# Kernel tuning notes

Measured on AMD Instinct MI355X. Metric: run time of the kernel, lower is better.

The kernel has to match this reference:

```python
import jax, jax.numpy as jnp
import numpy as np

E = 1024  # embedding_dim
QD = 1024  # query_dim (also key dim)
VD = 1024  # value_dim
B, S = 4, 2048


def setup_inputs() -> dict:
    key = jax.random.key(0)
    k1, k2, k3, k4, k5, k6, k7, k8 = jax.random.split(key, 8)
    x = jax.random.normal(k1, (B, S, E), dtype=jnp.float32)
    mask = jax.random.randint(k2, (B, S, S), 0, 2, dtype=jnp.int32)
    s = 1.0 / np.sqrt(E)
    Wq = jax.random.uniform(k3, (E, QD), jnp.float32, -s, s)
    bq = jax.random.uniform(k4, (QD,), jnp.float32, -s, s)
    Wk = jax.random.uniform(k5, (E, QD), jnp.float32, -s, s)
    bk = jax.random.uniform(k6, (QD,), jnp.float32, -s, s)
    Wv = jax.random.uniform(k7, (E, VD), jnp.float32, -s, s)
    bv = jax.random.uniform(k8, (VD,), jnp.float32, -s, s)
    return {"x": x, "mask": mask, "Wq": Wq, "bq": bq, "Wk": Wk, "bk": bk, "Wv": Wv, "bv": bv}


def reference(x, mask, Wq, bq, Wk, bk, Wv, bv):
    # projections: [B,S,E] @ [E,D] -> [B,S,D]
    q = jnp.einsum('bse,ed->bsd', x, Wq) + bq
    k = jnp.einsum('bse,ed->bsd', x, Wk) + bk
    v = jnp.einsum('bse,ed->bsd', x, Wv) + bv
    # scores scaled by query_dim (NOT sqrt(query_dim)), per original code
    weights = jnp.einsum('bqd,bkd->bqk', q, k) / QD
    weights = jnp.where(mask == 0, -jnp.inf, weights)
    weights = jax.nn.softmax(weights, axis=-1)
    out = jnp.einsum('bqk,bkd->bqd', weights, v)
    return out
```

## Files before the change

kernel.cpp:

```cpp
#include <hip/hip_runtime.h>
#include <hip/hip_bf16.h>


typedef __bf16 bf16x8 __attribute__((ext_vector_type(8)));
typedef __bf16 bf16x4 __attribute__((ext_vector_type(4)));
typedef float f32x4 __attribute__((ext_vector_type(4)));

#define BM 128
#define BN 128
#define BK 64

__device__ inline void glds16(const __bf16* g, __bf16* l) {
    __builtin_amdgcn_global_load_lds(
        (const __attribute__((address_space(1))) unsigned int*)g,
        (__attribute__((address_space(3))) unsigned int*)l,
        16, 0, 0);
}

template <int EPI>
__global__ __launch_bounds__(256) void gemm_bt(
    const __bf16* __restrict__ A, const __bf16* __restrict__ B,
    float* __restrict__ Cf, __bf16* __restrict__ Cb,
    const float* __restrict__ bias,
    int M, int N, int K, float scale,
    long sA, long sB, long sC)
{
    A += (long)blockIdx.z * sA;
    B += (long)blockIdx.z * sB;
    if (EPI == 3) Cf += (long)blockIdx.z * sC;
    if (EPI == 4) Cb += (long)blockIdx.z * sC;

    __shared__ __align__(16) char smraw[65536];
    float* smC = (float*)smraw;

    const int t = threadIdx.x;
    const int w = t >> 6;
    const int l = t & 63;
    const int row0 = blockIdx.x * BM;
    const int col0 = blockIdx.y * BN;
    const int wm = (w >> 1) * 64;
    const int wn = (w & 1) * 64;

    const int srow = l >> 3;
    const int skel = (((l & 7) ^ srow) & 7) * 8;

    const int lm = l & 15;
    const int g16 = l >> 4;
    const int sx = lm & 7;

    f32x4 acc[4][4];
#pragma unroll
    for (int i = 0; i < 4; i++)
#pragma unroll
        for (int j = 0; j < 4; j++) acc[i][j] = (f32x4){0.f, 0.f, 0.f, 0.f};

    auto stage = [&](int buf, int kt) {
        __bf16* sA = (__bf16*)(smraw + buf * 32768);
        __bf16* sB = sA + BM * BK;
#pragma unroll
        for (int i = 0; i < 4; i++) {
            const int chunk = i * 4 + w;
            const int r = chunk * 8 + srow;
            glds16(A + (size_t)(row0 + r) * K + kt + skel, &sA[chunk * 512]);
            glds16(B + (size_t)(col0 + r) * K + kt + skel, &sB[chunk * 512]);
        }
    };

    stage(0, 0);
    int cur = 0;
    for (int kt = 0; kt < K; kt += BK) {
        __syncthreads();
        if (kt + BK < K) stage(cur ^ 1, kt + BK);

        const __bf16* sA = (const __bf16*)(smraw + cur * 32768);
        const __bf16* sB = sA + BM * BK;
#pragma unroll
        for (int ks = 0; ks < 2; ks++) {
            bf16x8 af[4], bg[4];
            const int p = ((ks * 4 + g16) ^ sx) * 8;
#pragma unroll
            for (int mt = 0; mt < 4; mt++)
                af[mt] = *(const bf16x8*)&sA[(wm + mt * 16 + lm) * BK + p];
#pragma unroll
            for (int nt = 0; nt < 4; nt++)
                bg[nt] = *(const bf16x8*)&sB[(wn + nt * 16 + lm) * BK + p];
#pragma unroll
            for (int mt = 0; mt < 4; mt++)
#pragma unroll
                for (int nt = 0; nt < 4; nt++)
                    acc[mt][nt] = __builtin_amdgcn_mfma_f32_16x16x32_bf16(
                        af[mt], bg[nt], acc[mt][nt], 0, 0, 0);
        }
        cur ^= 1;
    }
    __syncthreads();

    const int rl = (l >> 4) * 4;
    float breg[4];
    if (EPI <= 1) {
#pragma unroll
        for (int nt = 0; nt < 4; nt++) breg[nt] = bias[col0 + wn + nt * 16 + lm];
    }
#pragma unroll
    for (int mt = 0; mt < 4; mt++) {
#pragma unroll
        for (int nt = 0; nt < 4; nt++)
#pragma unroll
            for (int i = 0; i < 4; i++) {
                const int lr = (w >> 1) * 16 + rl + i;
                const int c  = wn + nt * 16 + lm;
                float v = acc[mt][nt][i];
                if (EPI <= 1) v += breg[nt];
                if (EPI == 4) v *= scale;
                smC[lr * 132 + c] = v;
            }
        __syncthreads();

        if (EPI == 1) {
#pragma unroll
            for (int k = 0; k < 4; k++) {
                const int d  = (t >> 3) + 32 * k;
                const int sc = (t & 7) * 4;
                const int gr = row0 + mt * 16 + (sc & 15) + (sc >> 4) * 64;
                bf16x4 o;
#pragma unroll
                for (int j = 0; j < 4; j++) o[j] = (__bf16)smC[(sc + j) * 132 + d];
                *(bf16x4*)&Cb[(size_t)(gr >> 11) * ((size_t)N * 2048)
                              + (size_t)(col0 + d) * 2048 + (gr & 2047)] = o;
            }
        } else {
#pragma unroll
            for (int k = 0; k < 4; k++) {
                const int lr = (t >> 5) + 8 * k;
                const int c4 = (t & 31) * 4;
                const int gr = row0 + mt * 16 + (lr & 15) + (lr >> 4) * 64;
                const float4 v = *(const float4*)&smC[lr * 132 + c4];
                if (EPI == 0 || EPI == 4) {
                    bf16x4 o = {(__bf16)v.x, (__bf16)v.y, (__bf16)v.z, (__bf16)v.w};
                    *(bf16x4*)&Cb[(size_t)gr * N + col0 + c4] = o;
                } else {
                    *(float4*)&Cf[(size_t)gr * N + col0 + c4] = v;
                }
            }
        }
        __syncthreads();
    }
}

__global__ __launch_bounds__(256) void cast_x(const float* __restrict__ X, __bf16* __restrict__ Y) {
    const size_t i = (size_t)blockIdx.x * 256 + threadIdx.x;
    const float4* X4 = (const float4*)X;
    const float4 a = X4[i * 2], b = X4[i * 2 + 1];
    bf16x8 o = {(__bf16)a.x, (__bf16)a.y, (__bf16)a.z, (__bf16)a.w,
                (__bf16)b.x, (__bf16)b.y, (__bf16)b.z, (__bf16)b.w};
    ((bf16x8*)Y)[i] = o;
}

__global__ void cast_wt(const float* __restrict__ Wq, const float* __restrict__ Wk,
                        const float* __restrict__ Wv, __bf16* __restrict__ Wt) {
    const float* W = blockIdx.z == 0 ? Wq : (blockIdx.z == 1 ? Wk : Wv);
    __bf16* O = Wt + (size_t)blockIdx.z * 1024 * 1024;
    __shared__ float tile[32][33];
    const int tx = threadIdx.x, ty = threadIdx.y;
    const int d0 = blockIdx.x * 32, e0 = blockIdx.y * 32;
#pragma unroll
    for (int j = 0; j < 32; j += 8)
        tile[ty + j][tx] = W[(size_t)(e0 + ty + j) * 1024 + d0 + tx];
    __syncthreads();
#pragma unroll
    for (int j = 0; j < 32; j += 8)
        O[(size_t)(d0 + ty + j) * 1024 + e0 + tx] = (__bf16)tile[tx][ty + j];
}

__global__ __launch_bounds__(256) void softmax_rows(const __bf16* __restrict__ S,
                                                    const int* __restrict__ mask,
                                                    __bf16* __restrict__ P) {
    const size_t row = blockIdx.x;
    const int t = threadIdx.x;
    const int w = t >> 6, l = t & 63;
    const bf16x8 s8 = ((const bf16x8*)(S + row * 2048))[t];
    const int4 mk0 = ((const int4*)(mask + row * 2048))[t * 2];
    const int4 mk1 = ((const int4*)(mask + row * 2048))[t * 2 + 1];
    float v[8];
    v[0] = mk0.x ? (float)s8[0] : -1e30f;
    v[1] = mk0.y ? (float)s8[1] : -1e30f;
    v[2] = mk0.z ? (float)s8[2] : -1e30f;
    v[3] = mk0.w ? (float)s8[3] : -1e30f;
    v[4] = mk1.x ? (float)s8[4] : -1e30f;
    v[5] = mk1.y ? (float)s8[5] : -1e30f;
    v[6] = mk1.z ? (float)s8[6] : -1e30f;
    v[7] = mk1.w ? (float)s8[7] : -1e30f;
    float m = v[0];
#pragma unroll
    for (int i = 1; i < 8; i++) m = fmaxf(m, v[i]);
#pragma unroll
    for (int off = 32; off; off >>= 1) m = fmaxf(m, __shfl_xor(m, off, 64));
    __shared__ float rm[4], rs[4];
    if (l == 0) rm[w] = m;
    __syncthreads();
    m = fmaxf(fmaxf(rm[0], rm[1]), fmaxf(rm[2], rm[3]));
    float e[8], sum = 0.f;
#pragma unroll
    for (int i = 0; i < 8; i++) { e[i] = __expf(v[i] - m); sum += e[i]; }
#pragma unroll
    for (int off = 32; off; off >>= 1) sum += __shfl_xor(sum, off, 64);
    if (l == 0) rs[w] = sum;
    __syncthreads();
    const float inv = 1.f / (rs[0] + rs[1] + rs[2] + rs[3]);
    bf16x8 o;
#pragma unroll
    for (int i = 0; i < 8; i++) o[i] = (__bf16)(e[i] * inv);
    ((bf16x8*)(P + row * 2048))[t] = o;
}

extern "C" void kernel_launch(void* const* d_in, const int* in_sizes, int n_in,
                              void* d_out, int out_size, void* d_ws, size_t ws_size,
                              hipStream_t stream) {
    const float* x  = (const float*)d_in[0];
    const int* mask = (const int*)d_in[1];
    const float* Wq = (const float*)d_in[2];
    const float* bq = (const float*)d_in[3];
    const float* Wk = (const float*)d_in[4];
    const float* bk = (const float*)d_in[5];
    const float* Wv = (const float*)d_in[6];
    const float* bv = (const float*)d_in[7];
    float* out = (float*)d_out;

    char* ws = (char*)d_ws;
    __bf16* xb = (__bf16*)(ws);
    __bf16* Wt = (__bf16*)(ws + (16ull << 20));
    __bf16* Qb = (__bf16*)(ws + (22ull << 20));
    __bf16* Kb = (__bf16*)(ws + (38ull << 20));
    __bf16* Vt = (__bf16*)(ws + (54ull << 20));
    __bf16* Sf = (__bf16*)(ws + (70ull << 20));
    __bf16* Pb = (__bf16*)(ws + (22ull << 20));

    cast_x<<<4096, 256, 0, stream>>>(x, xb);
    cast_wt<<<dim3(32, 32, 3), dim3(32, 8), 0, stream>>>(Wq, Wk, Wv, Wt);

    gemm_bt<0><<<dim3(64, 8, 1), 256, 0, stream>>>(xb, Wt, nullptr, Qb, bq,
                                                   8192, 1024, 1024, 1.f, 0, 0, 0);
    gemm_bt<0><<<dim3(64, 8, 1), 256, 0, stream>>>(xb, Wt + (1u << 20), nullptr, Kb, bk,
                                                   8192, 1024, 1024, 1.f, 0, 0, 0);
    gemm_bt<1><<<dim3(64, 8, 1), 256, 0, stream>>>(xb, Wt + (2u << 20), nullptr, Vt, bv,
                                                   8192, 1024, 1024, 1.f, 0, 0, 0);

    gemm_bt<4><<<dim3(16, 16, 4), 256, 0, stream>>>(Qb, Kb, nullptr, Sf, nullptr,
                                                    2048, 2048, 1024, 1.0f / 1024.0f,
                                                    2048L * 1024, 2048L * 1024,
                                                    2048L * 2048);

    softmax_rows<<<8192, 256, 0, stream>>>(Sf, mask, Pb);

    gemm_bt<3><<<dim3(16, 8, 4), 256, 0, stream>>>(Pb, Vt, out, nullptr, nullptr,
                                                   2048, 1024, 2048, 1.f,
                                                   2048L * 2048, 1024L * 2048,
                                                   2048L * 1024);
}
```

Before: 299.0 us.

## Add 256x256-tile pipelined GEMM for fused QK projection and score GEMM

Introduces a new 512-thread GEMM kernel with 256x256 output tiles, a 128KB double-buffered LDS stage, swizzled LDS reads and an interleaved load/MFMA schedule that uses setprio and explicit waitcnts. It replaces the separate Q and K projection launches with a single launch that writes both outputs, and it also handles the QK^T score GEMM. The larger tiles raise arithmetic intensity and reduce global traffic per FLOP. The cost is that the grids get smaller (256 blocks), which may underfill the GPU's compute units, and the kernel relies on a fragile hand-tuned barrier/waitcnt schedule.

```diff
diff --git a/kernel.cpp b/kernel.cpp
--- a/kernel.cpp
+++ b/kernel.cpp
@@ -15,6 +15,166 @@
         (const __attribute__((address_space(1))) unsigned int*)g,
         (__attribute__((address_space(3))) unsigned int*)l,
         16, 0, 0);
+}
+
+template <int EPI>
+__global__ __launch_bounds__(512, 2) void gemm256(
+    const __bf16* __restrict__ A, const __bf16* __restrict__ B,
+    __bf16* __restrict__ C0, __bf16* __restrict__ C1,
+    const float* __restrict__ bias0, const float* __restrict__ bias1,
+    int K, int ldc, float scale, long sA, long sB, long sC)
+{
+    A += (long)blockIdx.z * sA;
+    B += (long)blockIdx.z * sB;
+
+    __shared__ __align__(16) char sm[131072];
+
+    const int t = threadIdx.x;
+    const int w = t >> 6, l = t & 63;
+    const int wm = w >> 2, wn = w & 3;
+    const int row0 = blockIdx.x * 256, col0 = blockIdx.y * 256;
+    const int srow = l >> 3;
+    const int skel = (((l & 7) ^ srow) & 7) * 8;
+    const int lm = l & 15, g16 = l >> 4, sx = lm & 7;
+
+    const __bf16* Ap = A + (size_t)row0 * K;
+    const __bf16* Bp = B + (size_t)col0 * K;
+
+    f32x4 acc[8][4];
+#pragma unroll
+    for (int i = 0; i < 8; i++)
+#pragma unroll
+        for (int j = 0; j < 4; j++) acc[i][j] = (f32x4){0.f, 0.f, 0.f, 0.f};
+
+    auto stageHalf = [&](int mat, int h, int buf, int kt) {
+        const __bf16* G = mat ? Bp : Ap;
+        char* base = sm + (buf << 16) + mat * 32768 + h * 16384;
+#pragma unroll
+        for (int i = 0; i < 2; i++) {
+            const int c = w * 2 + i;
+            glds16(G + (size_t)(h * 128 + c * 8 + srow) * K + kt + skel,
+                   (__bf16*)(base + c * 1024));
+        }
+    };
+
+    bf16x8 a03[4][2], a47[4][2], b01[2][2], b23[2][2];
+
+    auto rdA = [&](bf16x8 (&d)[4][2], int buf, int half) {
+        const char* Ab = sm + (buf << 16);
+#pragma unroll
+        for (int mt = 0; mt < 4; mt++) {
+            const int r = wm * 128 + half * 64 + mt * 16 + lm;
+#pragma unroll
+            for (int ks = 0; ks < 2; ks++)
+                d[mt][ks] = *(const bf16x8*)(Ab + r * 128 + ((((ks << 2) | g16) ^ sx) << 4));
+        }
+    };
+    auto rdB = [&](bf16x8 (&d)[2][2], int buf, int half) {
+        const char* Bb = sm + (buf << 16) + 32768;
+#pragma unroll
+        for (int nt = 0; nt < 2; nt++) {
+            const int r = wn * 64 + half * 32 + nt * 16 + lm;
+#pragma unroll
+            for (int ks = 0; ks < 2; ks++)
+                d[nt][ks] = *(const bf16x8*)(Bb + r * 128 + ((((ks << 2) | g16) ^ sx) << 4));
+        }
+    };
+    auto mf8 = [&](bf16x8 (&Af)[4][2], bf16x8 (&Bf)[2][2], int mo, int no) {
+#pragma unroll
+        for (int ks = 0; ks < 2; ks++)
+#pragma unroll
+            for (int mt = 0; mt < 4; mt++)
+#pragma unroll
+                for (int nt = 0; nt < 2; nt++)
+                    acc[mo + mt][no + nt] = __builtin_amdgcn_mfma_f32_16x16x32_bf16(
+                        Af[mt][ks], Bf[nt][ks], acc[mo + mt][no + nt], 0, 0, 0);
+    };
+
+#define BAR   __builtin_amdgcn_s_barrier()
+#define LGKM0 asm volatile("s_waitcnt lgkmcnt(0)" ::: "memory")
+#define VM4   asm volatile("s_waitcnt vmcnt(4)" ::: "memory")
+
+    stageHalf(0, 0, 0, 0); stageHalf(0, 1, 0, 0);
+    stageHalf(1, 0, 0, 0); stageHalf(1, 1, 0, 0);
+    stageHalf(0, 0, 1, 64); stageHalf(0, 1, 1, 64);
+    VM4; BAR;
+
+    const int nkt = K >> 6;
+    for (int tt = 0; tt < nkt; tt += 2) {
+#pragma unroll
+        for (int sub = 0; sub < 2; sub++) {
+            const int tcur = tt + sub;
+            const int buf = sub;
+            const int ktn1 = (tcur + 1) << 6;
+            const int ktn2 = (tcur + 2) << 6;
+            rdA(a03, buf, 0); rdB(b01, buf, 0);
+            stageHalf(1, 0, buf ^ 1, ktn1);
+            BAR; LGKM0;
+            __builtin_amdgcn_s_setprio(1); mf8(a03, b01, 0, 0); __builtin_amdgcn_s_setprio(0);
+            BAR;
+            rdA(a47, buf, 1); rdB(b23, buf, 1);
+            stageHalf(1, 1, buf ^ 1, ktn1);
+            BAR; LGKM0;
+            __builtin_amdgcn_s_setprio(1); mf8(a47, b01, 4, 0); __builtin_amdgcn_s_setprio(0);
+            BAR;
+            stageHalf(0, 0, buf, ktn2);
+            BAR; LGKM0;
+            __builtin_amdgcn_s_setprio(1); mf8(a03, b23, 0, 2); __builtin_amdgcn_s_setprio(0);
+            BAR;
+            stageHalf(0, 1, buf, ktn2);
+            BAR; LGKM0;
+            __builtin_amdgcn_s_setprio(1); mf8(a47, b23, 4, 2); __builtin_amdgcn_s_setprio(0);
+            VM4; BAR;
+        }
+    }
+#undef BAR
+#undef LGKM0
+#undef VM4
+
+    float* smC = (float*)sm;
+    const int rl = g16 * 4;
+    float breg[4];
+    __bf16* Cout;
+    int cbase;
+    if (EPI == 0) {
+        const bool isQ = (col0 < 1024);
+        const float* bias = isQ ? bias0 : bias1;
+        cbase = col0 & 1023;
+        Cout = isQ ? C0 : C1;
+#pragma unroll
+        for (int nt = 0; nt < 4; nt++) breg[nt] = bias[cbase + wn * 64 + nt * 16 + lm];
+    } else {
+        Cout = C0 + (long)blockIdx.z * sC;
+        cbase = col0;
+    }
+
+#pragma unroll
+    for (int mt = 0; mt < 8; mt++) {
+#pragma unroll
+        for (int nt = 0; nt < 4; nt++)
+#pragma unroll
+            for (int i = 0; i < 4; i++) {
+                const int lr = wm * 16 + rl + i;
+                const int c = wn * 64 + nt * 16 + lm;
+                float v = acc[mt][nt][i];
+                if (EPI == 0) v += breg[nt];
+                if (EPI == 4) v *= scale;
+                smC[lr * 260 + c] = v;
+            }
+        __syncthreads();
+        {
+            const int tr = t >> 4;
+            const int cc = (t & 15) * 16;
+            const int gr = row0 + (tr >> 4) * 128 + mt * 16 + (tr & 15);
+            const float* src = &smC[tr * 260 + cc];
+            bf16x8 o0, o1;
+#pragma unroll
+            for (int j = 0; j < 8; j++) { o0[j] = (__bf16)src[j]; o1[j] = (__bf16)src[8 + j]; }
+            *(bf16x8*)&Cout[(size_t)gr * ldc + cbase + cc] = o0;
+            *(bf16x8*)&Cout[(size_t)gr * ldc + cbase + cc + 8] = o1;
+        }
+        __syncthreads();
+    }
 }
 
 template <int EPI>
@@ -238,17 +398,15 @@
     cast_x<<<4096, 256, 0, stream>>>(x, xb);
     cast_wt<<<dim3(32, 32, 3), dim3(32, 8), 0, stream>>>(Wq, Wk, Wv, Wt);
 
-    gemm_bt<0><<<dim3(64, 8, 1), 256, 0, stream>>>(xb, Wt, nullptr, Qb, bq,
-                                                   8192, 1024, 1024, 1.f, 0, 0, 0);
-    gemm_bt<0><<<dim3(64, 8, 1), 256, 0, stream>>>(xb, Wt + (1u << 20), nullptr, Kb, bk,
-                                                   8192, 1024, 1024, 1.f, 0, 0, 0);
+    gemm256<0><<<dim3(32, 8, 1), 512, 0, stream>>>(xb, Wt, Qb, Kb, bq, bk,
+                                                   1024, 1024, 1.f, 0, 0, 0);
     gemm_bt<1><<<dim3(64, 8, 1), 256, 0, stream>>>(xb, Wt + (2u << 20), nullptr, Vt, bv,
                                                    8192, 1024, 1024, 1.f, 0, 0, 0);
 
-    gemm_bt<4><<<dim3(16, 16, 4), 256, 0, stream>>>(Qb, Kb, nullptr, Sf, nullptr,
-                                                    2048, 2048, 1024, 1.0f / 1024.0f,
-                                                    2048L * 1024, 2048L * 1024,
-                                                    2048L * 2048);
+    gemm256<4><<<dim3(8, 8, 4), 512, 0, stream>>>(Qb, Kb, Sf, nullptr, nullptr, nullptr,
+                                                  1024, 2048, 1.0f / 1024.0f,
+                                                  2048L * 1024, 2048L * 1024,
+                                                  2048L * 2048);
 
     softmax_rows<<<8192, 256, 0, stream>>>(Sf, mask, Pb);
 
```

Result: no change. 295.8 us (-1.1%).
